# Kernel optimization log

Measured on AMD Instinct MI355X. Metric: run time of the kernel, lower is better.

## Reference

```python
import jax, jax.numpy as jnp
import numpy as np

B, N, D, K = 16, 4096, 256, 2048  # batch, tokens, dim, codebook_size
COMMIT = 0.25

def setup_inputs() -> dict:
    key = jax.random.key(0)
    k1, k2 = jax.random.split(key)
    x = jax.random.normal(k1, (B, N, D), dtype=jnp.float32)
    # codebook buffer, stored as [dim, codebook_size] like lucidrains' VectorQuantize
    embed = jax.random.normal(k2, (D, K), dtype=jnp.float32)
    return {"x": x, "embed": embed}

def reference(x, embed):
    # flatten tokens: [B*N, D]
    flat = x.reshape(-1, D)
    # squared euclidean distance to every code: [B*N, K]
    dist = (jnp.sum(flat * flat, axis=1, keepdims=True)
            - 2.0 * (flat @ embed)
            + jnp.sum(embed * embed, axis=0, keepdims=True))
    idx = jnp.argmin(dist, axis=1)          # nearest code per token, [B*N]
    indices = idx.reshape(B, N)
    quantize = embed.T[indices]             # gather codes -> [B, N, D]
    # commitment loss: mse(quantize.detach(), x) * commitment
    commit_loss = jnp.mean(jnp.square(jax.lax.stop_gradient(quantize) - x)) * COMMIT
    # straight-through estimator
    quantize = x + jax.lax.stop_gradient(quantize - x)
    return quantize, commit_loss, indices
```

## Files before the change

kernel.cpp:

```cpp
#include <hip/hip_runtime.h>

#define TOK   65536
#define DIMS  256
#define NCODE 2048
#define LOSSOFF 16777216
#define IDXOFF  16777217

typedef _Float16 f16x8 __attribute__((ext_vector_type(8)));
typedef _Float16 f16x4 __attribute__((ext_vector_type(4)));
typedef float    f32x4 __attribute__((ext_vector_type(4)));

__device__ __forceinline__ void ld16(void* lds, const void* g) {
  __builtin_amdgcn_global_load_lds(
      (const __attribute__((address_space(1))) unsigned int*)g,
      (__attribute__((address_space(3))) unsigned int*)lds, 16, 0, 0);
}
__device__ __forceinline__ unsigned long long umin64(unsigned long long a,
                                                     unsigned long long b) {
  return a < b ? a : b;
}

__global__ void k_prep(const float* __restrict__ embed, float* __restrict__ embedT,
                       _Float16* __restrict__ eTh, _Float16* __restrict__ eTl) {
  __shared__ float t[32][33];
  int tx = threadIdx.x & 31, ty = threadIdx.x >> 5;
  int k0 = blockIdx.x * 32, d0 = blockIdx.y * 32;
#pragma unroll
  for (int i = 0; i < 4; ++i) {
    int d = ty + i * 8;
    t[tx][d] = embed[(size_t)(d0 + d) * NCODE + k0 + tx];
  }
  __syncthreads();
#pragma unroll
  for (int i = 0; i < 4; ++i) {
    int kl = ty + i * 8;
    float v = t[kl][tx];
    size_t o = (size_t)(k0 + kl) * DIMS + d0 + tx;
    embedT[o] = v;
    _Float16 h = (_Float16)v;
    eTh[o] = h;
    eTl[o] = (_Float16)(v - (float)h);
  }
}

__global__ void k_e2(const float* __restrict__ embed, float* __restrict__ e2) {
  int k = blockIdx.x * 256 + threadIdx.x;
  double a = 0.0;
  for (int d = 0; d < DIMS; ++d) {
    float v = embed[(size_t)d * NCODE + k];
    a += (double)v * (double)v;
  }
  e2[k] = (float)a;
}

__global__ void k_xsplit(const float* __restrict__ x, _Float16* __restrict__ xh,
                         _Float16* __restrict__ xl,
                         unsigned long long* __restrict__ part,
                         float* __restrict__ out) {
  int gid = blockIdx.x * 256 + threadIdx.x;
  if (gid < TOK) part[gid] = ~0ull;
  if (gid == 0) out[LOSSOFF] = 0.0f;
  size_t base = (size_t)gid;
#pragma unroll
  for (int i = 0; i < 8; ++i) {
    size_t o = (base + (size_t)i * 524288) * 4;
    f32x4 v = *(const f32x4*)&x[o];
    f16x4 h, l;
#pragma unroll
    for (int e = 0; e < 4; ++e) {
      h[e] = (_Float16)v[e];
      l[e] = (_Float16)(v[e] - (float)h[e]);
    }
    *(f16x4*)&xh[o] = h;
    *(f16x4*)&xl[o] = l;
  }
}

#define MM(ah_, al_, bh_, bl_, a_) do { \
  a_ = __builtin_amdgcn_mfma_f32_16x16x32_f16(ah_, bh_, a_, 0, 0, 0); \
  a_ = __builtin_amdgcn_mfma_f32_16x16x32_f16(ah_, bl_, a_, 0, 0, 0); \
  a_ = __builtin_amdgcn_mfma_f32_16x16x32_f16(al_, bh_, a_, 0, 0, 0); } while (0)

#define SBAR_PRE do { __builtin_amdgcn_sched_barrier(0); __builtin_amdgcn_s_barrier(); \
  asm volatile("s_waitcnt lgkmcnt(0)" ::: "memory"); __builtin_amdgcn_sched_barrier(0); \
  __builtin_amdgcn_s_setprio(1); } while (0)

#define SBAR_POST do { __builtin_amdgcn_s_setprio(0); __builtin_amdgcn_sched_barrier(0); \
  __builtin_amdgcn_s_barrier(); } while (0)

__global__ __launch_bounds__(512, 1) void k_score(
    const _Float16* __restrict__ xh, const _Float16* __restrict__ xl,
    const _Float16* __restrict__ eTh, const _Float16* __restrict__ eTl,
    const float* __restrict__ e2, unsigned long long* __restrict__ part) {
  __shared__ __attribute__((aligned(16))) _Float16 Ah[3][256 * 32];
  __shared__ __attribute__((aligned(16))) _Float16 Al[3][256 * 32];
  __shared__ __attribute__((aligned(16))) _Float16 Bh[3][128 * 32];
  __shared__ __attribute__((aligned(16))) _Float16 Bl[3][128 * 32];

  int tid = threadIdx.x, lane = tid & 63, wid = tid >> 6;
  int wm = wid >> 1, wn = wid & 1;
  int bid = blockIdx.x;
  int wg = (bid & 7) * 512 + (bid >> 3);
  int mblk = wg >> 4, nblk = wg & 15;
  int t0 = mblk * 256, c0 = nblk * 128;
  int col = lane & 15, kg = lane >> 4;

  f32x4 acc[4][4] = {};

  auto stageA = [&](int ck, int slot) {
    int kb = ck * 32;
#pragma unroll
    for (int q = 0; q < 2; ++q) {
      int i = q * 512 + wid * 64 + lane;
      int row = i >> 2;
      int g = (i & 3) ^ ((row >> 1) & 3);
      size_t src = (size_t)(t0 + row) * DIMS + kb + g * 8;
      ld16(&Ah[slot][(q * 512 + wid * 64) * 8], &xh[src]);
      ld16(&Al[slot][(q * 512 + wid * 64) * 8], &xl[src]);
    }
  };
  auto stageB = [&](int ck, int slot) {
    int kb = ck * 32;
    int i = wid * 64 + lane;
    int row = i >> 2;
    int g = (i & 3) ^ ((row >> 1) & 3);
    size_t src = (size_t)(c0 + row) * DIMS + kb + g * 8;
    ld16(&Bh[slot][(wid * 64) * 8], &eTh[src]);
    ld16(&Bl[slot][(wid * 64) * 8], &eTl[src]);
  };
  auto rdA = [&](int slot, int mf, f16x8& h, f16x8& l) {
    int row = wm * 64 + mf * 16 + col;
    int off = row * 32 + (kg ^ ((row >> 1) & 3)) * 8;
    h = *(const f16x8*)&Ah[slot][off];
    l = *(const f16x8*)&Al[slot][off];
  };
  auto rdB = [&](int slot, int nf, f16x8& h, f16x8& l) {
    int row = wn * 64 + nf * 16 + col;
    int off = row * 32 + (kg ^ ((row >> 1) & 3)) * 8;
    h = *(const f16x8*)&Bh[slot][off];
    l = *(const f16x8*)&Bl[slot][off];
  };

  stageA(0, 0); stageB(0, 0);
  stageA(1, 1); stageB(1, 1);
  asm volatile("s_waitcnt vmcnt(6)" ::: "memory");
  __builtin_amdgcn_sched_barrier(0);
  __builtin_amdgcn_s_barrier();

#pragma unroll
  for (int c = 0; c < 8; ++c) {
    int slot = c % 3;
    f16x8 a0h, a0l, a1h, a1l, a2h, a2l, a3h, a3l;
    f16x8 b0h, b0l, b1h, b1l, b2h, b2l, b3h, b3l;
    if (c < 6) stageA(c + 2, (c + 2) % 3);
    rdA(slot, 0, a0h, a0l); rdA(slot, 1, a1h, a1l);
    rdB(slot, 0, b0h, b0l); rdB(slot, 1, b1h, b1l);
    SBAR_PRE;
    MM(a0h, a0l, b0h, b0l, acc[0][0]); MM(a0h, a0l, b1h, b1l, acc[0][1]);
    MM(a1h, a1l, b0h, b0l, acc[1][0]); MM(a1h, a1l, b1h, b1l, acc[1][1]);
    SBAR_POST;
    if (c < 6) stageB(c + 2, (c + 2) % 3);
    rdB(slot, 2, b2h, b2l); rdB(slot, 3, b3h, b3l);
    SBAR_PRE;
    MM(a0h, a0l, b2h, b2l, acc[0][2]); MM(a0h, a0l, b3h, b3l, acc[0][3]);
    MM(a1h, a1l, b2h, b2l, acc[1][2]); MM(a1h, a1l, b3h, b3l, acc[1][3]);
    SBAR_POST;
    rdA(slot, 2, a2h, a2l); rdA(slot, 3, a3h, a3l);
    SBAR_PRE;
    MM(a2h, a2l, b0h, b0l, acc[2][0]); MM(a2h, a2l, b1h, b1l, acc[2][1]);
    MM(a3h, a3l, b0h, b0l, acc[3][0]); MM(a3h, a3l, b1h, b1l, acc[3][1]);
    SBAR_POST;
    SBAR_PRE;
    MM(a2h, a2l, b2h, b2l, acc[2][2]); MM(a2h, a2l, b3h, b3l, acc[2][3]);
    MM(a3h, a3l, b2h, b2l, acc[3][2]); MM(a3h, a3l, b3h, b3l, acc[3][3]);
    __builtin_amdgcn_s_setprio(0);
    __builtin_amdgcn_sched_barrier(0);
    if (c < 6) {
      asm volatile("s_waitcnt vmcnt(6)" ::: "memory");
    } else if (c == 6) {
      asm volatile("s_waitcnt vmcnt(0)" ::: "memory");
    }
    __builtin_amdgcn_sched_barrier(0);
    if (c < 7) __builtin_amdgcn_s_barrier();
  }

  float e2n[4];
#pragma unroll
  for (int n = 0; n < 4; ++n) e2n[n] = e2[c0 + wn * 64 + n * 16 + col];
#pragma unroll
  for (int m = 0; m < 4; ++m)
#pragma unroll
    for (int r = 0; r < 4; ++r) {
      unsigned long long best = ~0ull;
#pragma unroll
      for (int n = 0; n < 4; ++n) {
        float s = e2n[n] - 2.0f * acc[m][n][r];
        unsigned u = __float_as_uint(s);
        u ^= (u & 0x80000000u) ? 0xFFFFFFFFu : 0x80000000u;
        best = umin64(best, ((unsigned long long)u << 32) |
                            (unsigned)(c0 + wn * 64 + n * 16 + col));
      }
#pragma unroll
      for (int off = 1; off < 16; off <<= 1)
        best = umin64(best, __shfl_xor(best, off, 64));
      if (col == 0)
        atomicMin(&part[t0 + wm * 64 + m * 16 + kg * 4 + r], best);
    }
}

__global__ void k_gather(const float* __restrict__ x, const float* __restrict__ embedT,
                         const unsigned long long* __restrict__ part,
                         float* __restrict__ out) {
  int wid = threadIdx.x >> 6, lane = threadIdx.x & 63;
  int gw = blockIdx.x * 4 + wid;
  float s = 0.0f;
#pragma unroll
  for (int t = 0; t < 8; ++t) {
    int token = gw * 8 + t;
    int code = (int)(part[token] & 0xFFFFFFFFull);
    if (lane == 0) out[IDXOFF + token] = (float)code;
    f32x4 q  = *(const f32x4*)&embedT[(size_t)code * DIMS + lane * 4];
    f32x4 xv = *(const f32x4*)&x[(size_t)token * DIMS + lane * 4];
    f32x4 d = q - xv;
    *(f32x4*)&out[(size_t)token * DIMS + lane * 4] = xv + d;
    s += d[0] * d[0] + d[1] * d[1] + d[2] * d[2] + d[3] * d[3];
  }
  for (int off = 32; off; off >>= 1) s += __shfl_xor(s, off, 64);
  __shared__ float red[4];
  if (lane == 0) red[wid] = s;
  __syncthreads();
  if (threadIdx.x == 0) {
    float tsum = (red[0] + red[1] + red[2] + red[3]) * (0.25f / 16777216.0f);
    atomicAdd(&out[LOSSOFF], tsum);
  }
}

extern "C" void kernel_launch(void* const* d_in, const int* in_sizes, int n_in,
                              void* d_out, int out_size, void* d_ws, size_t ws_size,
                              hipStream_t stream) {
  const float* x     = (const float*)d_in[0];
  const float* embed = (const float*)d_in[1];
  float* out = (float*)d_out;
  _Float16* xh = (_Float16*)d_out;
  _Float16* xl = (_Float16*)((char*)d_out + (32u << 20));
  char* w = (char*)d_ws;
  _Float16* eTh    = (_Float16*)w;
  _Float16* eTl    = (_Float16*)(w + (1u << 20));
  float*    embedT = (float*)(w + (2u << 20));
  float*    e2     = (float*)(w + (4u << 20));
  unsigned long long* part = (unsigned long long*)(w + (4u << 20) + (1u << 15));

  hipLaunchKernelGGL(k_prep,   dim3(NCODE / 32, DIMS / 32), dim3(256), 0, stream, embed, embedT, eTh, eTl);
  hipLaunchKernelGGL(k_e2,     dim3(NCODE / 256),           dim3(256), 0, stream, embed, e2);
  hipLaunchKernelGGL(k_xsplit, dim3(2048),                  dim3(256), 0, stream, x, xh, xl, part, out);
  hipLaunchKernelGGL(k_score,  dim3(4096),                  dim3(512), 0, stream, xh, xl, eTh, eTl, e2, part);
  hipLaunchKernelGGL(k_gather, dim3(2048),                  dim3(256), 0, stream, x, embedT, part, out);
}
```

Measured before the change: 554.3 us.

## Replace ping-pong barrier phases with a single read-then-MFMA block per K chunk

```diff
diff --git a/kernel.cpp b/kernel.cpp
--- a/kernel.cpp
+++ b/kernel.cpp
@@ -81,13 +81,6 @@
   a_ = __builtin_amdgcn_mfma_f32_16x16x32_f16(ah_, bl_, a_, 0, 0, 0); \
   a_ = __builtin_amdgcn_mfma_f32_16x16x32_f16(al_, bh_, a_, 0, 0, 0); } while (0)
 
-#define SBAR_PRE do { __builtin_amdgcn_sched_barrier(0); __builtin_amdgcn_s_barrier(); \
-  asm volatile("s_waitcnt lgkmcnt(0)" ::: "memory"); __builtin_amdgcn_sched_barrier(0); \
-  __builtin_amdgcn_s_setprio(1); } while (0)
-
-#define SBAR_POST do { __builtin_amdgcn_s_setprio(0); __builtin_amdgcn_sched_barrier(0); \
-  __builtin_amdgcn_s_barrier(); } while (0)
-
 __global__ __launch_bounds__(512, 1) void k_score(
     const _Float16* __restrict__ xh, const _Float16* __restrict__ xl,
     const _Float16* __restrict__ eTh, const _Float16* __restrict__ eTl,
@@ -146,33 +139,25 @@
   asm volatile("s_waitcnt vmcnt(6)" ::: "memory");
   __builtin_amdgcn_sched_barrier(0);
   __builtin_amdgcn_s_barrier();
+  __builtin_amdgcn_sched_barrier(0);
 
 #pragma unroll
   for (int c = 0; c < 8; ++c) {
     int slot = c % 3;
-    f16x8 a0h, a0l, a1h, a1l, a2h, a2l, a3h, a3l;
-    f16x8 b0h, b0l, b1h, b1l, b2h, b2l, b3h, b3l;
-    if (c < 6) stageA(c + 2, (c + 2) % 3);
-    rdA(slot, 0, a0h, a0l); rdA(slot, 1, a1h, a1l);
-    rdB(slot, 0, b0h, b0l); rdB(slot, 1, b1h, b1l);
-    SBAR_PRE;
-    MM(a0h, a0l, b0h, b0l, acc[0][0]); MM(a0h, a0l, b1h, b1l, acc[0][1]);
-    MM(a1h, a1l, b0h, b0l, acc[1][0]); MM(a1h, a1l, b1h, b1l, acc[1][1]);
-    SBAR_POST;
-    if (c < 6) stageB(c + 2, (c + 2) % 3);
-    rdB(slot, 2, b2h, b2l); rdB(slot, 3, b3h, b3l);
-    SBAR_PRE;
-    MM(a0h, a0l, b2h, b2l, acc[0][2]); MM(a0h, a0l, b3h, b3l, acc[0][3]);
-    MM(a1h, a1l, b2h, b2l, acc[1][2]); MM(a1h, a1l, b3h, b3l, acc[1][3]);
-    SBAR_POST;
-    rdA(slot, 2, a2h, a2l); rdA(slot, 3, a3h, a3l);
-    SBAR_PRE;
-    MM(a2h, a2l, b0h, b0l, acc[2][0]); MM(a2h, a2l, b1h, b1l, acc[2][1]);
-    MM(a3h, a3l, b0h, b0l, acc[3][0]); MM(a3h, a3l, b1h, b1l, acc[3][1]);
-    SBAR_POST;
-    SBAR_PRE;
-    MM(a2h, a2l, b2h, b2l, acc[2][2]); MM(a2h, a2l, b3h, b3l, acc[2][3]);
-    MM(a3h, a3l, b2h, b2l, acc[3][2]); MM(a3h, a3l, b3h, b3l, acc[3][3]);
+    f16x8 ah[4], al[4], bh[4], bl[4];
+#pragma unroll
+    for (int m = 0; m < 4; ++m) rdA(slot, m, ah[m], al[m]);
+#pragma unroll
+    for (int n = 0; n < 4; ++n) rdB(slot, n, bh[n], bl[n]);
+    __builtin_amdgcn_sched_barrier(0);
+    if (c < 6) { stageA(c + 2, (c + 2) % 3); stageB(c + 2, (c + 2) % 3); }
+    __builtin_amdgcn_sched_barrier(0);
+    __builtin_amdgcn_s_setprio(1);
+#pragma unroll
+    for (int m = 0; m < 4; ++m)
+#pragma unroll
+      for (int n = 0; n < 4; ++n)
+        MM(ah[m], al[m], bh[n], bl[n], acc[m][n]);
     __builtin_amdgcn_s_setprio(0);
     __builtin_amdgcn_sched_barrier(0);
     if (c < 6) {
@@ -182,6 +167,7 @@
     }
     __builtin_amdgcn_sched_barrier(0);
     if (c < 7) __builtin_amdgcn_s_barrier();
+    __builtin_amdgcn_sched_barrier(0);
   }
 
   float e2n[4];
```

After: 508.5 us. 8.3% less time.
